# Kernel tuning notes

Measured on AMD Instinct MI355X. Metric: run time of the kernel, lower is better.

## Reference

```python
import jax, jax.numpy as jnp
import numpy as np

D_MODEL = 1024
NUM_HEADS = 16
HEAD_DIM = D_MODEL // NUM_HEADS
EPS = 1e-06


def setup_inputs() -> dict:
    key = jax.random.key(0)
    ks = jax.random.split(key, 7)
    B, T, D = 4, 4096, D_MODEL
    scale = 1.0 / np.sqrt(D)
    x = jax.random.normal(ks[0], (B, T, D), dtype=jnp.float32)
    Wq = jax.random.normal(ks[1], (D, D), dtype=jnp.float32) * scale
    Wk = jax.random.normal(ks[2], (D, D), dtype=jnp.float32) * scale
    Wv = jax.random.normal(ks[3], (D, D), dtype=jnp.float32) * scale
    Wo = jax.random.normal(ks[4], (D, D), dtype=jnp.float32) * scale
    Wg = jax.random.normal(ks[5], (D, D), dtype=jnp.float32) * scale
    bg = jnp.zeros((D,), dtype=jnp.float32)
    return {"x": x, "Wq": Wq, "Wk": Wk, "Wv": Wv, "Wo": Wo, "Wg": Wg, "bg": bg}


def phi(x):
    return jax.nn.elu(x) + 1.0


def reference(x, Wq, Wk, Wv, Wo, Wg, bg):
    B, T, D = x.shape
    H, Hd = NUM_HEADS, HEAD_DIM
    # torch nn.Linear: y = x @ W.T
    q = phi((x @ Wq.T).reshape(B, T, H, Hd))
    k = phi((x @ Wk.T).reshape(B, T, H, Hd))
    v = (x @ Wv.T).reshape(B, T, H, Hd)
    k_sum = k.sum(axis=1)                              # [B,H,Hd]
    kv_sum = jnp.einsum('bthd,bthd->bhd', k, v)        # [B,H,Hd] (elementwise-product reduction, as in source)
    # out[b,t,h,v] = sum_d q[b,t,h,d]*kv_sum[b,h,d], identical for every v
    s = jnp.einsum('bthd,bhd->bth', q, kv_sum)         # [B,T,H]
    z = jnp.einsum('bthd,bhd->bth', q, k_sum) + EPS    # [B,T,H]
    out = (s / z)[..., None] * jnp.ones((Hd,), dtype=x.dtype)  # broadcast over head_dim
    out = out.reshape(B, T, D)
    gate = jax.nn.sigmoid(x @ Wg.T + bg)
    return gate * out + (1.0 - gate) * x
```

## Files before the change

kernel.cpp:

```cpp
#include <hip/hip_runtime.h>

#define D_MODEL 1024
#define TSEQ    4096
#define BATCH   4
#define MROWS   (BATCH * TSEQ)
#define KDIM    1024
#define NDIM    1024
#define EPSV    1e-6f

typedef __attribute__((ext_vector_type(8))) short short8;
typedef __attribute__((ext_vector_type(4))) float floatx4;

__device__ inline unsigned short f2bf(float f) {
  unsigned u = __float_as_uint(f);
  unsigned r = (u + 0x7FFFu + ((u >> 16) & 1u)) >> 16;
  return (unsigned short)r;
}
__device__ inline float bf2f(unsigned short h) {
  return __uint_as_float(((unsigned)h) << 16);
}
__device__ inline float phi_f(float x) { return x > 0.f ? x + 1.f : __expf(x); }

#define GLD16(gp, lp) __builtin_amdgcn_global_load_lds( \
    (const __attribute__((address_space(1))) void*)(gp), \
    (__attribute__((address_space(3))) void*)(lp), 16, 0, 0)

#define NX4 4194304
#define NW4 262144
#define NZ4 2048

__global__ __launch_bounds__(256) void prep_kernel(
    const float* __restrict__ x,  const float* __restrict__ wq,
    const float* __restrict__ wk, const float* __restrict__ wv,
    const float* __restrict__ wg,
    unsigned short* __restrict__ xb,  unsigned short* __restrict__ wqb,
    unsigned short* __restrict__ wkb, unsigned short* __restrict__ wvb,
    unsigned short* __restrict__ wgb, float* __restrict__ zbase)
{
  long i = (long)blockIdx.x * 256 + threadIdx.x;
  const float* src; unsigned short* dst; long j = i;
  if (j < NX4) { src = x; dst = xb; }
  else {
    j -= NX4;
    if (j < NW4) { src = wq; dst = wqb; }
    else { j -= NW4;
      if (j < NW4) { src = wk; dst = wkb; }
      else { j -= NW4;
        if (j < NW4) { src = wv; dst = wvb; }
        else { j -= NW4;
          if (j < NW4) { src = wg; dst = wgb; }
          else { j -= NW4;
            if (j < NZ4) { float4 zz = {0.f,0.f,0.f,0.f}; ((float4*)zbase)[j] = zz; }
            return;
          }
        }
      }
    }
  }
  float4 f = ((const float4*)src)[j];
  ushort4 o;
  o.x = f2bf(f.x); o.y = f2bf(f.y); o.z = f2bf(f.z); o.w = f2bf(f.w);
  ((ushort4*)dst)[j] = o;
}

#define BM 128
#define BN 128
#define BK 32

__global__ __launch_bounds__(256, 2) void gemm_kv_kernel(
    const unsigned short* __restrict__ A,
    const unsigned short* __restrict__ Wk, const unsigned short* __restrict__ Wv,
    float* __restrict__ ksum, float* __restrict__ kvsum)
{
  const int bn = blockIdx.x;
  const int bm = blockIdx.y;

  __shared__ __align__(16) unsigned short As [2][BM * BK];
  __shared__ __align__(16) unsigned short Bks[2][BN * BK];
  __shared__ __align__(16) unsigned short Bvs[2][BN * BK];

  const int tid  = threadIdx.x;
  const int lane = tid & 63;
  const int w    = tid >> 6;
  const int wr   = (w >> 1) * 64;
  const int wc   = (w & 1) * 64;

  floatx4 ak[4][4], av[4][4];
#pragma unroll
  for (int i = 0; i < 4; i++)
#pragma unroll
    for (int j = 0; j < 4; j++) {
      floatx4 zz = {0.f,0.f,0.f,0.f}; ak[i][j] = zz; av[i][j] = zz;
    }

  const unsigned short* Ablk  = A  + (size_t)bm * BM * KDIM;
  const unsigned short* Bkblk = Wk + (size_t)bn * BN * KDIM;
  const unsigned short* Bvblk = Wv + (size_t)bn * BN * KDIM;

  const int la = lane & 15;
  const int lk = (lane >> 4) * 8;

  const int f0 = tid;
  const int f1 = tid + 256;
  const int r0 = f0 >> 2, c0 = (f0 & 3) * 8;
  const int r1 = f1 >> 2, c1 = (f1 & 3) * 8;

  auto stage = [&](int buf, int kt) {
    size_t g0 = (size_t)r0 * KDIM + kt + c0;
    size_t g1 = (size_t)r1 * KDIM + kt + c1;
    GLD16(Ablk  + g0, &As [buf][f0 * 8]); GLD16(Ablk  + g1, &As [buf][f1 * 8]);
    GLD16(Bkblk + g0, &Bks[buf][f0 * 8]); GLD16(Bkblk + g1, &Bks[buf][f1 * 8]);
    GLD16(Bvblk + g0, &Bvs[buf][f0 * 8]); GLD16(Bvblk + g1, &Bvs[buf][f1 * 8]);
  };

  auto compute = [&](int buf) {
    short8 af[4], bk[4], bv[4];
#pragma unroll
    for (int i = 0; i < 4; i++) {
      af[i] = *(const short8*)&As [buf][(wr + i * 16 + la) * BK + lk];
      bk[i] = *(const short8*)&Bks[buf][(wc + i * 16 + la) * BK + lk];
      bv[i] = *(const short8*)&Bvs[buf][(wc + i * 16 + la) * BK + lk];
    }
    __builtin_amdgcn_s_setprio(1);
#pragma unroll
    for (int i = 0; i < 4; i++)
#pragma unroll
      for (int j = 0; j < 4; j++) {
        ak[i][j] = __builtin_amdgcn_mfma_f32_16x16x32_bf16(af[i], bk[j], ak[i][j], 0, 0, 0);
        av[i][j] = __builtin_amdgcn_mfma_f32_16x16x32_bf16(af[i], bv[j], av[i][j], 0, 0, 0);
      }
    __builtin_amdgcn_s_setprio(0);
  };

  stage(0, 0);
  __syncthreads();
  for (int kt = 0; kt < KDIM; kt += 2 * BK) {
    stage(1, kt + BK);
    compute(0);
    __syncthreads();
    if (kt + 2 * BK < KDIM) stage(0, kt + 2 * BK);
    compute(1);
    __syncthreads();
  }

  const int b = bm >> 5;
  float kp[4] = {0.f,0.f,0.f,0.f};
  float vp[4] = {0.f,0.f,0.f,0.f};
#pragma unroll
  for (int j = 0; j < 4; j++)
#pragma unroll
    for (int i = 0; i < 4; i++)
#pragma unroll
      for (int r = 0; r < 4; r++) {
        float kk = phi_f(ak[i][j][r]);
        kp[j] += kk;
        vp[j] += kk * av[i][j][r];
      }
#pragma unroll
  for (int j = 0; j < 4; j++) {
    kp[j] += __shfl_xor(kp[j], 16, 64); kp[j] += __shfl_xor(kp[j], 32, 64);
    vp[j] += __shfl_xor(vp[j], 16, 64); vp[j] += __shfl_xor(vp[j], 32, 64);
  }
  if (lane < 16) {
#pragma unroll
    for (int j = 0; j < 4; j++) {
      int col = bn * BN + wc + j * 16 + lane;
      atomicAdd(ksum  + (size_t)b * D_MODEL + col, kp[j]);
      atomicAdd(kvsum + (size_t)b * D_MODEL + col, vp[j]);
    }
  }
}

__global__ __launch_bounds__(512) void gemm_qg_kernel(
    const unsigned short* __restrict__ A,
    const unsigned short* __restrict__ Wq, const unsigned short* __restrict__ Wg,
    const float* __restrict__ x, const float* __restrict__ bg,
    const float* __restrict__ ksum, const float* __restrict__ kvsum,
    float* __restrict__ out)
{
  const int bn = blockIdx.x;
  const int bm = blockIdx.y;

  __shared__ __align__(16) unsigned short As [2][BM * BK];
  __shared__ __align__(16) unsigned short Bqs[2][BN * BK];
  __shared__ __align__(16) unsigned short Bgs[2][BN * BK];
  __shared__ float o_lds[2 * BM];

  const int tid  = threadIdx.x;
  const int lane = tid & 63;
  const int w    = tid >> 6;
  const int is_g = w >> 2;
  const int wl   = w & 3;
  const int wr   = (wl >> 1) * 64;
  const int wc   = (wl & 1) * 64;

  floatx4 acc[4][4];
#pragma unroll
  for (int i = 0; i < 4; i++)
#pragma unroll
    for (int j = 0; j < 4; j++) { floatx4 zz = {0.f,0.f,0.f,0.f}; acc[i][j] = zz; }

  const unsigned short* Ablk  = A + (size_t)bm * BM * KDIM;
  const unsigned short* Bqblk = Wq + (size_t)bn * BN * KDIM;
  const unsigned short* Bgblk = Wg + (size_t)bn * BN * KDIM;

  const int la = lane & 15;
  const int lk = (lane >> 4) * 8;

  const int f  = tid;
  const int rr = f >> 2, cc = (f & 3) * 8;

  auto stage = [&](int buf, int kt) {
    size_t g = (size_t)rr * KDIM + kt + cc;
    GLD16(Ablk  + g, &As [buf][f * 8]);
    GLD16(Bqblk + g, &Bqs[buf][f * 8]);
    GLD16(Bgblk + g, &Bgs[buf][f * 8]);
  };

  auto compute = [&](int buf) {
    const unsigned short* Bsm = is_g ? &Bgs[buf][0] : &Bqs[buf][0];
    short8 af[4], bfg[4];
#pragma unroll
    for (int i = 0; i < 4; i++) {
      af[i]  = *(const short8*)&As[buf][(wr + i * 16 + la) * BK + lk];
      bfg[i] = *(const short8*)&Bsm[(wc + i * 16 + la) * BK + lk];
    }
    __builtin_amdgcn_s_setprio(1);
#pragma unroll
    for (int i = 0; i < 4; i++)
#pragma unroll
      for (int j = 0; j < 4; j++)
        acc[i][j] = __builtin_amdgcn_mfma_f32_16x16x32_bf16(af[i], bfg[j], acc[i][j], 0, 0, 0);
    __builtin_amdgcn_s_setprio(0);
  };

  stage(0, 0);
  __syncthreads();
  for (int kt = 0; kt < KDIM; kt += 2 * BK) {
    stage(1, kt + BK);
    compute(0);
    __syncthreads();
    if (kt + 2 * BK < KDIM) stage(0, kt + 2 * BK);
    compute(1);
    __syncthreads();
  }

  const int b  = bm >> 5;
  const int ro = (lane >> 4) * 4;
  const int co = lane & 15;
  const int hl = wc >> 6;

  if (!is_g) {
    float kvv[4], ksv[4];
#pragma unroll
    for (int j = 0; j < 4; j++) {
      int col = bn * BN + wc + j * 16 + co;
      kvv[j] = kvsum[(size_t)b * D_MODEL + col];
      ksv[j] = ksum [(size_t)b * D_MODEL + col];
    }
#pragma unroll
    for (int i = 0; i < 4; i++)
#pragma unroll
      for (int r = 0; r < 4; r++) {
        float s = 0.f, z = 0.f;
#pragma unroll
        for (int j = 0; j < 4; j++) {
          float qq = phi_f(acc[i][j][r]);
          s += qq * kvv[j]; z += qq * ksv[j];
        }
#pragma unroll
        for (int m = 1; m < 16; m <<= 1) {
          s += __shfl_xor(s, m, 64);
          z += __shfl_xor(z, m, 64);
        }
        if (co == 0) o_lds[hl * BM + wr + i * 16 + ro + r] = s / (z + EPSV);
      }
  }
  __syncthreads();
  if (is_g) {
    float bgv[4];
#pragma unroll
    for (int j = 0; j < 4; j++) bgv[j] = bg[bn * BN + wc + j * 16 + co];
#pragma unroll
    for (int i = 0; i < 4; i++)
#pragma unroll
      for (int r = 0; r < 4; r++) {
        int rowl = wr + i * 16 + ro + r;
        int grow = bm * BM + rowl;
        float ov = o_lds[hl * BM + rowl];
#pragma unroll
        for (int j = 0; j < 4; j++) {
          int gcol = bn * BN + wc + j * 16 + co;
          float gt = 1.f / (1.f + __expf(-(acc[i][j][r] + bgv[j])));
          float xv = x[(size_t)grow * D_MODEL + gcol];
          out[(size_t)grow * D_MODEL + gcol] = gt * ov + (1.f - gt) * xv;
        }
      }
  }
}

extern "C" void kernel_launch(void* const* d_in, const int* in_sizes, int n_in,
                              void* d_out, int out_size, void* d_ws, size_t ws_size,
                              hipStream_t stream) {
  (void)in_sizes; (void)n_in; (void)out_size; (void)ws_size;
  const float* x  = (const float*)d_in[0];
  const float* Wq = (const float*)d_in[1];
  const float* Wk = (const float*)d_in[2];
  const float* Wv = (const float*)d_in[3];
  const float* Wg = (const float*)d_in[5];
  const float* bg = (const float*)d_in[6];
  float* out = (float*)d_out;

  char* ws = (char*)d_ws;
  const size_t xel = (size_t)MROWS * D_MODEL;
  const size_t wel = (size_t)NDIM * KDIM;
  unsigned short* xbf = (unsigned short*)ws; ws += xel * 2;
  unsigned short* wqb = (unsigned short*)ws; ws += wel * 2;
  unsigned short* wkb = (unsigned short*)ws; ws += wel * 2;
  unsigned short* wvb = (unsigned short*)ws; ws += wel * 2;
  unsigned short* wgb = (unsigned short*)ws; ws += wel * 2;
  float* ksum  = (float*)ws; ws += (size_t)BATCH * D_MODEL * 4;
  float* kvsum = (float*)ws; ws += (size_t)BATCH * D_MODEL * 4;

  const long total4 = (long)NX4 + 4L * NW4 + NZ4;
  prep_kernel<<<(int)((total4 + 255) / 256), 256, 0, stream>>>(
      x, Wq, Wk, Wv, Wg, xbf, wqb, wkb, wvb, wgb, ksum);

  dim3 g1(NDIM / BN, MROWS / BM);
  gemm_kv_kernel<<<g1, 256, 0, stream>>>(xbf, wkb, wvb, ksum, kvsum);

  dim3 g2(NDIM / BN, MROWS / BM);
  gemm_qg_kernel<<<g2, 512, 0, stream>>>(xbf, wqb, wgb, x, bg, ksum, kvsum, out);
}
```

Before: 293.1 us.

## Enlarge GEMM tiles to 256x128x64 with XOR-swizzled LDS and split-stage pipelining

Result: faster. 278.5 us (-5.0%).

```diff
diff --git a/kernel.cpp b/kernel.cpp
--- a/kernel.cpp
+++ b/kernel.cpp
@@ -15,9 +15,6 @@
   unsigned u = __float_as_uint(f);
   unsigned r = (u + 0x7FFFu + ((u >> 16) & 1u)) >> 16;
   return (unsigned short)r;
-}
-__device__ inline float bf2f(unsigned short h) {
-  return __uint_as_float(((unsigned)h) << 16);
 }
 __device__ inline float phi_f(float x) { return x > 0.f ? x + 1.f : __expf(x); }
 
@@ -63,107 +60,144 @@
   ((ushort4*)dst)[j] = o;
 }
 
-#define BM 128
+#define BM 256
 #define BN 128
-#define BK 32
-
-__global__ __launch_bounds__(256, 2) void gemm_kv_kernel(
+#define BK 64
+#define NSTEP (KDIM / BK)
+
+
+__global__ __launch_bounds__(512, 1) void gemm_kv_kernel(
     const unsigned short* __restrict__ A,
     const unsigned short* __restrict__ Wk, const unsigned short* __restrict__ Wv,
     float* __restrict__ ksum, float* __restrict__ kvsum)
 {
-  const int bn = blockIdx.x;
-  const int bm = blockIdx.y;
-
-  __shared__ __align__(16) unsigned short As [2][BM * BK];
-  __shared__ __align__(16) unsigned short Bks[2][BN * BK];
-  __shared__ __align__(16) unsigned short Bvs[2][BN * BK];
+  __shared__ __align__(16) unsigned short As0[BM * BK], As1[BM * BK];
+  __shared__ __align__(16) unsigned short Bk0[BN * BK], Bk1[BN * BK];
+  __shared__ __align__(16) unsigned short Bv0[BN * BK], Bv1[BN * BK];
+
+  const int bid = blockIdx.x;
+  const int sw  = (bid & 7) * 64 + (bid >> 3);
+  const int bn  = sw & 7;
+  const int bm  = sw >> 3;
 
   const int tid  = threadIdx.x;
   const int lane = tid & 63;
   const int w    = tid >> 6;
-  const int wr   = (w >> 1) * 64;
-  const int wc   = (w & 1) * 64;
-
-  floatx4 ak[4][4], av[4][4];
-#pragma unroll
-  for (int i = 0; i < 4; i++)
-#pragma unroll
-    for (int j = 0; j < 4; j++) {
+  const int wr   = (w >> 2) * 128;
+  const int wc   = (w & 3) * 32;
+  const int la   = lane & 15;
+  const int l4   = lane >> 4;
+
+  floatx4 ak[8][2], av[8][2];
+#pragma unroll
+  for (int i = 0; i < 8; i++)
+#pragma unroll
+    for (int j = 0; j < 2; j++) {
       floatx4 zz = {0.f,0.f,0.f,0.f}; ak[i][j] = zz; av[i][j] = zz;
     }
 
-  const unsigned short* Ablk  = A  + (size_t)bm * BM * KDIM;
-  const unsigned short* Bkblk = Wk + (size_t)bn * BN * KDIM;
-  const unsigned short* Bvblk = Wv + (size_t)bn * BN * KDIM;
-
-  const int la = lane & 15;
-  const int lk = (lane >> 4) * 8;
-
-  const int f0 = tid;
-  const int f1 = tid + 256;
-  const int r0 = f0 >> 2, c0 = (f0 & 3) * 8;
-  const int r1 = f1 >> 2, c1 = (f1 & 3) * 8;
-
-  auto stage = [&](int buf, int kt) {
-    size_t g0 = (size_t)r0 * KDIM + kt + c0;
-    size_t g1 = (size_t)r1 * KDIM + kt + c1;
-    GLD16(Ablk  + g0, &As [buf][f0 * 8]); GLD16(Ablk  + g1, &As [buf][f1 * 8]);
-    GLD16(Bkblk + g0, &Bks[buf][f0 * 8]); GLD16(Bkblk + g1, &Bks[buf][f1 * 8]);
-    GLD16(Bvblk + g0, &Bvs[buf][f0 * 8]); GLD16(Bvblk + g1, &Bvs[buf][f1 * 8]);
+  const unsigned short* Ablk = A  + (size_t)bm * BM * KDIM;
+  const unsigned short* Bkb  = Wk + (size_t)bn * BN * KDIM;
+  const unsigned short* Bvb  = Wv + (size_t)bn * BN * KDIM;
+
+  auto stage_half = [&](unsigned short* Aw, unsigned short* Bkw, unsigned short* Bvw,
+                        int kt, int half) {
+#pragma unroll
+    for (int j = 0; j < 2; ++j) {
+      int s = tid + (half * 2 + j) * 512;
+      int row = s >> 3, sl = s & 7;
+      size_t g = (size_t)row * KDIM + kt + ((sl ^ (row & 7)) << 3);
+      GLD16(Ablk + g, Aw + (size_t)s * 8);
+    }
+    {
+      int s = tid + half * 512;
+      int row = s >> 3, sl = s & 7;
+      size_t g = (size_t)row * KDIM + kt + ((sl ^ (row & 7)) << 3);
+      GLD16(Bkb + g, Bkw + (size_t)s * 8);
+      GLD16(Bvb + g, Bvw + (size_t)s * 8);
+    }
   };
 
-  auto compute = [&](int buf) {
-    short8 af[4], bk[4], bv[4];
-#pragma unroll
-    for (int i = 0; i < 4; i++) {
-      af[i] = *(const short8*)&As [buf][(wr + i * 16 + la) * BK + lk];
-      bk[i] = *(const short8*)&Bks[buf][(wc + i * 16 + la) * BK + lk];
-      bv[i] = *(const short8*)&Bvs[buf][(wc + i * 16 + la) * BK + lk];
-    }
-    __builtin_amdgcn_s_setprio(1);
-#pragma unroll
-    for (int i = 0; i < 4; i++)
-#pragma unroll
-      for (int j = 0; j < 4; j++) {
-        ak[i][j] = __builtin_amdgcn_mfma_f32_16x16x32_bf16(af[i], bk[j], ak[i][j], 0, 0, 0);
-        av[i][j] = __builtin_amdgcn_mfma_f32_16x16x32_bf16(af[i], bv[j], av[i][j], 0, 0, 0);
-      }
-    __builtin_amdgcn_s_setprio(0);
+  auto kstep = [&](const unsigned short* Ar, const unsigned short* Bkr,
+                   const unsigned short* Bvr,
+                   unsigned short* Aw, unsigned short* Bkw, unsigned short* Bvw,
+                   int ktn, bool pre) {
+    short8 bkf[2][2], bvf[2][2];
+#pragma unroll
+    for (int p = 0; p < 4; ++p) {
+      short8 af[2][2];
+#pragma unroll
+      for (int rp = 0; rp < 2; ++rp)
+#pragma unroll
+        for (int kk = 0; kk < 2; ++kk) {
+          int row  = wr + (2 * p + rp) * 16 + la;
+          int slot = kk * 4 + l4;
+          af[rp][kk] = *(const short8*)(Ar + row * BK + ((slot ^ (row & 7)) << 3));
+        }
+      if (p == 0) {
+#pragma unroll
+        for (int j = 0; j < 2; ++j)
+#pragma unroll
+          for (int kk = 0; kk < 2; ++kk) {
+            int row  = wc + j * 16 + la;
+            int slot = kk * 4 + l4;
+            int off  = row * BK + ((slot ^ (row & 7)) << 3);
+            bkf[j][kk] = *(const short8*)(Bkr + off);
+            bvf[j][kk] = *(const short8*)(Bvr + off);
+          }
+      }
+      if (p == 0 && pre) stage_half(Aw, Bkw, Bvw, ktn, 0);
+      if (p == 1 && pre) stage_half(Aw, Bkw, Bvw, ktn, 1);
+      __builtin_amdgcn_s_barrier();
+      __builtin_amdgcn_s_setprio(1);
+#pragma unroll
+      for (int rp = 0; rp < 2; ++rp)
+#pragma unroll
+        for (int j = 0; j < 2; ++j)
+#pragma unroll
+          for (int kk = 0; kk < 2; ++kk) {
+            ak[2*p+rp][j] = __builtin_amdgcn_mfma_f32_16x16x32_bf16(
+                af[rp][kk], bkf[j][kk], ak[2*p+rp][j], 0, 0, 0);
+            av[2*p+rp][j] = __builtin_amdgcn_mfma_f32_16x16x32_bf16(
+                af[rp][kk], bvf[j][kk], av[2*p+rp][j], 0, 0, 0);
+          }
+      __builtin_amdgcn_s_setprio(0);
+      if (p == 3) asm volatile("s_waitcnt vmcnt(0)" ::: "memory");
+      __builtin_amdgcn_s_barrier();
+    }
   };
 
-  stage(0, 0);
-  __syncthreads();
-  for (int kt = 0; kt < KDIM; kt += 2 * BK) {
-    stage(1, kt + BK);
-    compute(0);
-    __syncthreads();
-    if (kt + 2 * BK < KDIM) stage(0, kt + 2 * BK);
-    compute(1);
-    __syncthreads();
-  }
-
-  const int b = bm >> 5;
-  float kp[4] = {0.f,0.f,0.f,0.f};
-  float vp[4] = {0.f,0.f,0.f,0.f};
-#pragma unroll
-  for (int j = 0; j < 4; j++)
-#pragma unroll
-    for (int i = 0; i < 4; i++)
+  stage_half(As0, Bk0, Bv0, 0, 0);
+  stage_half(As0, Bk0, Bv0, 0, 1);
+  asm volatile("s_waitcnt vmcnt(0)" ::: "memory");
+  __builtin_amdgcn_s_barrier();
+
+  for (int st2 = 0; st2 < NSTEP; st2 += 2) {
+    kstep(As0, Bk0, Bv0, As1, Bk1, Bv1, (st2 + 1) * BK, true);
+    kstep(As1, Bk1, Bv1, As0, Bk0, Bv0, (st2 + 2) * BK, st2 + 2 < NSTEP);
+  }
+
+  const int b = bm >> 4;
+  float kp[2] = {0.f, 0.f};
+  float vp[2] = {0.f, 0.f};
+#pragma unroll
+  for (int j = 0; j < 2; j++)
+#pragma unroll
+    for (int mi = 0; mi < 8; mi++)
 #pragma unroll
       for (int r = 0; r < 4; r++) {
-        float kk = phi_f(ak[i][j][r]);
+        float kk = phi_f(ak[mi][j][r]);
         kp[j] += kk;
-        vp[j] += kk * av[i][j][r];
-      }
-#pragma unroll
-  for (int j = 0; j < 4; j++) {
+        vp[j] += kk * av[mi][j][r];
+      }
+#pragma unroll
+  for (int j = 0; j < 2; j++) {
     kp[j] += __shfl_xor(kp[j], 16, 64); kp[j] += __shfl_xor(kp[j], 32, 64);
     vp[j] += __shfl_xor(vp[j], 16, 64); vp[j] += __shfl_xor(vp[j], 32, 64);
   }
   if (lane < 16) {
 #pragma unroll
-    for (int j = 0; j < 4; j++) {
+    for (int j = 0; j < 2; j++) {
       int col = bn * BN + wc + j * 16 + lane;
       atomicAdd(ksum  + (size_t)b * D_MODEL + col, kp[j]);
       atomicAdd(kvsum + (size_t)b * D_MODEL + col, vp[j]);
@@ -171,83 +205,119 @@
   }
 }
 
-__global__ __launch_bounds__(512) void gemm_qg_kernel(
+__global__ __launch_bounds__(512, 1) void gemm_qg_kernel(
     const unsigned short* __restrict__ A,
     const unsigned short* __restrict__ Wq, const unsigned short* __restrict__ Wg,
     const float* __restrict__ x, const float* __restrict__ bg,
     const float* __restrict__ ksum, const float* __restrict__ kvsum,
     float* __restrict__ out)
 {
-  const int bn = blockIdx.x;
-  const int bm = blockIdx.y;
-
-  __shared__ __align__(16) unsigned short As [2][BM * BK];
-  __shared__ __align__(16) unsigned short Bqs[2][BN * BK];
-  __shared__ __align__(16) unsigned short Bgs[2][BN * BK];
+  __shared__ __align__(16) unsigned short As0[BM * BK], As1[BM * BK];
+  __shared__ __align__(16) unsigned short Bq0[BN * BK], Bq1[BN * BK];
+  __shared__ __align__(16) unsigned short Bg0[BN * BK], Bg1[BN * BK];
   __shared__ float o_lds[2 * BM];
+
+  const int bid = blockIdx.x;
+  const int sw  = (bid & 7) * 64 + (bid >> 3);
+  const int bn  = sw & 7;
+  const int bm  = sw >> 3;
 
   const int tid  = threadIdx.x;
   const int lane = tid & 63;
   const int w    = tid >> 6;
   const int is_g = w >> 2;
   const int wl   = w & 3;
-  const int wr   = (wl >> 1) * 64;
+  const int wr   = (wl >> 1) * 128;
   const int wc   = (wl & 1) * 64;
-
-  floatx4 acc[4][4];
-#pragma unroll
-  for (int i = 0; i < 4; i++)
+  const int la   = lane & 15;
+  const int l4   = lane >> 4;
+
+  floatx4 acc[8][4];
+#pragma unroll
+  for (int i = 0; i < 8; i++)
 #pragma unroll
     for (int j = 0; j < 4; j++) { floatx4 zz = {0.f,0.f,0.f,0.f}; acc[i][j] = zz; }
 
-  const unsigned short* Ablk  = A + (size_t)bm * BM * KDIM;
-  const unsigned short* Bqblk = Wq + (size_t)bn * BN * KDIM;
-  const unsigned short* Bgblk = Wg + (size_t)bn * BN * KDIM;
-
-  const int la = lane & 15;
-  const int lk = (lane >> 4) * 8;
-
-  const int f  = tid;
-  const int rr = f >> 2, cc = (f & 3) * 8;
-
-  auto stage = [&](int buf, int kt) {
-    size_t g = (size_t)rr * KDIM + kt + cc;
-    GLD16(Ablk  + g, &As [buf][f * 8]);
-    GLD16(Bqblk + g, &Bqs[buf][f * 8]);
-    GLD16(Bgblk + g, &Bgs[buf][f * 8]);
+  const unsigned short* Ablk = A  + (size_t)bm * BM * KDIM;
+  const unsigned short* Bqb  = Wq + (size_t)bn * BN * KDIM;
+  const unsigned short* Bgb  = Wg + (size_t)bn * BN * KDIM;
+
+  auto stage_half = [&](unsigned short* Aw, unsigned short* Bqw, unsigned short* Bgw,
+                        int kt, int half) {
+#pragma unroll
+    for (int j = 0; j < 2; ++j) {
+      int s = tid + (half * 2 + j) * 512;
+      int row = s >> 3, sl = s & 7;
+      size_t g = (size_t)row * KDIM + kt + ((sl ^ (row & 7)) << 3);
+      GLD16(Ablk + g, Aw + (size_t)s * 8);
+    }
+    {
+      int s = tid + half * 512;
+      int row = s >> 3, sl = s & 7;
+      size_t g = (size_t)row * KDIM + kt + ((sl ^ (row & 7)) << 3);
+      GLD16(Bqb + g, Bqw + (size_t)s * 8);
+      GLD16(Bgb + g, Bgw + (size_t)s * 8);
+    }
   };
 
-  auto compute = [&](int buf) {
-    const unsigned short* Bsm = is_g ? &Bgs[buf][0] : &Bqs[buf][0];
-    short8 af[4], bfg[4];
-#pragma unroll
-    for (int i = 0; i < 4; i++) {
-      af[i]  = *(const short8*)&As[buf][(wr + i * 16 + la) * BK + lk];
-      bfg[i] = *(const short8*)&Bsm[(wc + i * 16 + la) * BK + lk];
-    }
-    __builtin_amdgcn_s_setprio(1);
-#pragma unroll
-    for (int i = 0; i < 4; i++)
-#pragma unroll
-      for (int j = 0; j < 4; j++)
-        acc[i][j] = __builtin_amdgcn_mfma_f32_16x16x32_bf16(af[i], bfg[j], acc[i][j], 0, 0, 0);
-    __builtin_amdgcn_s_setprio(0);
+  auto kstep = [&](const unsigned short* Ar, const unsigned short* Bqr,
+                   const unsigned short* Bgr,
+                   unsigned short* Aw, unsigned short* Bqw, unsigned short* Bgw,
+                   int ktn, bool pre) {
+    const unsigned short* Br = is_g ? Bgr : Bqr;
+    short8 bf[4][2];
+#pragma unroll
+    for (int p = 0; p < 4; ++p) {
+      short8 af[2][2];
+#pragma unroll
+      for (int rp = 0; rp < 2; ++rp)
+#pragma unroll
+        for (int kk = 0; kk < 2; ++kk) {
+          int row  = wr + (2 * p + rp) * 16 + la;
+          int slot = kk * 4 + l4;
+          af[rp][kk] = *(const short8*)(Ar + row * BK + ((slot ^ (row & 7)) << 3));
+        }
+      if (p == 0) {
+#pragma unroll
+        for (int j = 0; j < 4; ++j)
+#pragma unroll
+          for (int kk = 0; kk < 2; ++kk) {
+            int row  = wc + j * 16 + la;
+            int slot = kk * 4 + l4;
+            bf[j][kk] = *(const short8*)(Br + row * BK + ((slot ^ (row & 7)) << 3));
+          }
+      }
+      if (p == 0 && pre) stage_half(Aw, Bqw, Bgw, ktn, 0);
+      if (p == 1 && pre) stage_half(Aw, Bqw, Bgw, ktn, 1);
+      __builtin_amdgcn_s_barrier();
+      __builtin_amdgcn_s_setprio(1);
+#pragma unroll
+      for (int rp = 0; rp < 2; ++rp)
+#pragma unroll
+        for (int j = 0; j < 4; ++j)
+#pragma unroll
+          for (int kk = 0; kk < 2; ++kk)
+            acc[2*p+rp][j] = __builtin_amdgcn_mfma_f32_16x16x32_bf16(
+                af[rp][kk], bf[j][kk], acc[2*p+rp][j], 0, 0, 0);
+      __builtin_amdgcn_s_setprio(0);
+      if (p == 3) asm volatile("s_waitcnt vmcnt(0)" ::: "memory");
+      __builtin_amdgcn_s_barrier();
+    }
   };
 
-  stage(0, 0);
-  __syncthreads();
-  for (int kt = 0; kt < KDIM; kt += 2 * BK) {
-    stage(1, kt + BK);
-    compute(0);
-    __syncthreads();
-    if (kt + 2 * BK < KDIM) stage(0, kt + 2 * BK);
-    compute(1);
-    __syncthreads();
-  }
-
-  const int b  = bm >> 5;
-  const int ro = (lane >> 4) * 4;
-  const int co = lane & 15;
+  stage_half(As0, Bq0, Bg0, 0, 0);
+  stage_half(As0, Bq0, Bg0, 0, 1);
+  asm volatile("s_waitcnt vmcnt(0)" ::: "memory");
+  __builtin_amdgcn_s_barrier();
+
+  for (int st2 = 0; st2 < NSTEP; st2 += 2) {
+    kstep(As0, Bq0, Bg0, As1, Bq1, Bg1, (st2 + 1) * BK, true);
+    kstep(As1, Bq1, Bg1, As0, Bq0, Bg0, (st2 + 2) * BK, st2 + 2 < NSTEP);
+  }
+
+  const int b  = bm >> 4;
+  const int ro = l4 * 4;
+  const int co = la;
   const int hl = wc >> 6;
 
   if (!is_g) {
@@ -259,13 +329,13 @@
       ksv[j] = ksum [(size_t)b * D_MODEL + col];
     }
 #pragma unroll
-    for (int i = 0; i < 4; i++)
+    for (int mi = 0; mi < 8; mi++)
 #pragma unroll
       for (int r = 0; r < 4; r++) {
         float s = 0.f, z = 0.f;
 #pragma unroll
         for (int j = 0; j < 4; j++) {
-          float qq = phi_f(acc[i][j][r]);
+          float qq = phi_f(acc[mi][j][r]);
           s += qq * kvv[j]; z += qq * ksv[j];
         }
 #pragma unroll
@@ -273,7 +343,7 @@
           s += __shfl_xor(s, m, 64);
           z += __shfl_xor(z, m, 64);
         }
-        if (co == 0) o_lds[hl * BM + wr + i * 16 + ro + r] = s / (z + EPSV);
+        if (co == 0) o_lds[hl * BM + wr + mi * 16 + ro + r] = s / (z + EPSV);
       }
   }
   __syncthreads();
@@ -282,16 +352,16 @@
 #pragma unroll
     for (int j = 0; j < 4; j++) bgv[j] = bg[bn * BN + wc + j * 16 + co];
 #pragma unroll
-    for (int i = 0; i < 4; i++)
+    for (int mi = 0; mi < 8; mi++)
 #pragma unroll
       for (int r = 0; r < 4; r++) {
-        int rowl = wr + i * 16 + ro + r;
+        int rowl = wr + mi * 16 + ro + r;
         int grow = bm * BM + rowl;
         float ov = o_lds[hl * BM + rowl];
 #pragma unroll
         for (int j = 0; j < 4; j++) {
           int gcol = bn * BN + wc + j * 16 + co;
-          float gt = 1.f / (1.f + __expf(-(acc[i][j][r] + bgv[j])));
+          float gt = 1.f / (1.f + __expf(-(acc[mi][j][r] + bgv[j])));
           float xv = x[(size_t)grow * D_MODEL + gcol];
           out[(size_t)grow * D_MODEL + gcol] = gt * ov + (1.f - gt) * xv;
         }
@@ -326,9 +396,7 @@
   prep_kernel<<<(int)((total4 + 255) / 256), 256, 0, stream>>>(
       x, Wq, Wk, Wv, Wg, xbf, wqb, wkb, wvb, wgb, ksum);
 
-  dim3 g1(NDIM / BN, MROWS / BM);
-  gemm_kv_kernel<<<g1, 256, 0, stream>>>(xbf, wkb, wvb, ksum, kvsum);
-
-  dim3 g2(NDIM / BN, MROWS / BM);
-  gemm_qg_kernel<<<g2, 512, 0, stream>>>(xbf, wqb, wgb, x, bg, ksum, kvsum, out);
+  gemm_kv_kernel<<<512, 512, 0, stream>>>(xbf, wkb, wvb, ksum, kvsum);
+
+  gemm_qg_kernel<<<512, 512, 0, stream>>>(xbf, wqb, wgb, x, bg, ksum, kvsum, out);
 }
```
